# Optimization experiments

Measured on AMD Instinct MI355X. Metric: run time of the kernel, lower is better.

The kernel has to match this reference:

```python
import jax, jax.numpy as jnp
import numpy as np

B, NC, NS = 128, 32, 128          # graphs, compound atoms/graph, pocket sites/graph
NV, NSITE = B * NC, B * NS        # 4096 compound atoms, 16384 site atoms total
EV, ES = NV * 4, NSITE * 8        # edge counts (avg degree 4 / 8)
FDIM, SDIM = 82, 32               # atom feature dims
H, HS, HP, HI = 128, 128, 128, 64 # hidden_vert, hidden_site, hidden_prot, hidden_int
D, K = 3, 8                       # GNN depth (both), attention heads
P = B * NC * NS                   # 524288 site-atom pairs


def setup_inputs():
    key = jax.random.key(0)
    ks = iter(jax.random.split(key, 80))
    def nrm(shape, s=0.05):
        return jax.random.normal(next(ks), shape, jnp.float32) * s
    inp = {}
    inp['x_vert'] = jax.random.normal(next(ks), (NV, FDIM), jnp.float32)
    inp['vert_src'] = jax.random.randint(next(ks), (EV,), 0, NV)
    inp['vert_dst'] = jax.random.randint(next(ks), (EV,), 0, NV)
    inp['vert_batch'] = jnp.repeat(jnp.arange(B, dtype=jnp.int32), NC)
    inp['W_emb'] = nrm((FDIM, H)); inp['b_emb'] = jnp.zeros((H,), jnp.float32)
    inp['Wa_main'] = nrm((D, K, H, H)); inp['Wa_super'] = nrm((D, K, H, H))
    inp['Wv'] = nrm((D, K, H, H)); inp['Wb'] = nrm((D, K, H))
    inp['Wm2s'] = nrm((D, K * H, H)); inp['Ws2m'] = nrm((D, H, H))
    inp['Wsup'] = nrm((D, H, H)); inp['Wself'] = nrm((D, H, H))
    inp['Wzm1'] = nrm((D, H, H)); inp['Wzm2'] = nrm((D, H, H))
    inp['Wzs1'] = nrm((D, H, H)); inp['Wzs2'] = nrm((D, H, H))
    for tag in ('m', 's'):
        inp['Wih_' + tag] = nrm((H, 3 * H)); inp['Whh_' + tag] = nrm((H, 3 * H))
        inp['bih_' + tag] = jnp.zeros((3 * H,), jnp.float32)
        inp['bhh_' + tag] = jnp.zeros((3 * H,), jnp.float32)
    inp['x_site'] = jax.random.normal(next(ks), (NSITE, SDIM), jnp.float32)
    inp['site_src'] = jax.random.randint(next(ks), (ES,), 0, NSITE)
    inp['site_dst'] = jax.random.randint(next(ks), (ES,), 0, NSITE)
    inp['W0'] = nrm((2 * SDIM, HS)); inp['b0'] = jnp.zeros((HS,), jnp.float32)
    inp['Wconv'] = nrm((D - 1, 2 * HS, HS)); inp['bconv'] = jnp.zeros((D - 1, HS), jnp.float32)
    inp['Wout'] = nrm((SDIM + D * HS, HP)); inp['bout'] = jnp.zeros((HP,), jnp.float32)
    inp['Wis'] = nrm((7, HP, HI)); inp['bis'] = jnp.zeros((7, HI), jnp.float32)
    inp['Wic'] = nrm((7, H, HI)); inp['bic'] = jnp.zeros((7, HI), jnp.float32)
    # block-diagonal all-pairs index (every site x every compound atom within a graph)
    g = jnp.arange(B, dtype=jnp.int32)
    a = jnp.arange(NS, dtype=jnp.int32)
    c = jnp.arange(NC, dtype=jnp.int32)
    inp['idx_site'] = jnp.broadcast_to(g[:, None, None] * NS + a[None, :, None], (B, NS, NC)).reshape(-1)
    inp['idx_comp'] = jnp.broadcast_to(g[:, None, None] * NC + c[None, None, :], (B, NS, NC)).reshape(-1)
    return inp


def _leaky(x):
    return jnp.where(x > 0, x, 0.1 * x)


def _gru(x, h, Wih, Whh, bih, bhh):
    gi = x @ Wih + bih
    gh = h @ Whh + bhh
    ir, iz, inn = jnp.split(gi, 3, axis=-1)
    hr, hz, hn = jnp.split(gh, 3, axis=-1)
    r = jax.nn.sigmoid(ir + hr)
    z = jax.nn.sigmoid(iz + hz)
    n = jnp.tanh(inn + r * hn)
    return (1.0 - z) * n + z * h


def reference(x_vert, vert_src, vert_dst, vert_batch, W_emb, b_emb,
              Wa_main, Wa_super, Wv, Wb, Wm2s, Ws2m, Wsup, Wself,
              Wzm1, Wzm2, Wzs1, Wzs2,
              Wih_m, Whh_m, bih_m, bhh_m, Wih_s, Whh_s, bih_s, bhh_s,
              x_site, site_src, site_dst, W0, b0, Wconv, bconv, Wout, bout,
              Wis, bis, Wic, bic, idx_site, idx_comp):
    seg = jax.ops.segment_sum
    # ---- GraphConv_module: embedding + GWM (graph warp) iterations ----
    vert = _leaky(x_vert @ W_emb + b_emb)                      # [NV, H]
    supe = seg(vert, vert_batch, num_segments=B)               # [B, H] super node init
    for d in range(D):
        # local vertex message passing
        nei = seg(vert[vert_src], vert_dst, num_segments=NV)
        main_self = _leaky((vert + nei) @ Wself[d])
        # multi-head main -> super attention (segment softmax over each graph)
        am = jnp.tanh(jnp.einsum('nd,kde->kne', vert, Wa_main[d]))        # [K,NV,H]
        asup = jnp.tanh(jnp.einsum('bd,kde->kbe', supe, Wa_super[d]))     # [K,B,H]
        score = jnp.einsum('kne,ke->nk', am * asup[:, vert_batch], Wb[d]) # [NV,K]
        smax = jax.ops.segment_max(score, vert_batch, num_segments=B)
        e = jnp.exp(score - smax[vert_batch])
        attn = e / seg(e, vert_batch, num_segments=B)[vert_batch]         # [NV,K]
        msg = jnp.einsum('nd,kde->nke', vert, Wv[d])                      # [NV,K,H]
        m2s = seg(attn[:, :, None] * msg, vert_batch, num_segments=B)     # [B,K,H]
        main_to_super = jnp.tanh(m2s.reshape(B, K * H) @ Wm2s[d])         # [B,H]
        super_to_main = jnp.tanh(supe @ Ws2m[d])[vert_batch]              # [NV,H]
        # warp gates + shared GRU updates
        zm = jax.nn.sigmoid(main_self @ Wzm1[d] + super_to_main @ Wzm2[d])
        vert = _gru((1 - zm) * main_self + zm * super_to_main, vert, Wih_m, Whh_m, bih_m, bhh_m)
        super_self = jnp.tanh(supe @ Wsup[d])
        zs = jax.nn.sigmoid(super_self @ Wzs1[d] + main_to_super @ Wzs2[d])
        supe = _gru((1 - zs) * super_self + zs * main_to_super, supe, Wih_s, Whh_s, bih_s, bhh_s)
    # ---- AtomConv_module on protein sites ----
    h = x_site
    feats = [h]
    for i in range(D):
        nei = seg(h[site_src], site_dst, num_segments=NSITE)
        W = W0 if i == 0 else Wconv[i - 1]
        b = b0 if i == 0 else bconv[i - 1]
        h = _leaky(jnp.concatenate([h, nei], axis=-1) @ W + b)
        feats.append(h)
    site = _leaky(jnp.concatenate(feats, axis=-1) @ Wout + bout)  # [NSITE, HP]
    # ---- Interaction_pred_module: 7-head gather-multiply-reduce over pairs ----
    preds = []
    for i in range(7):
        pa = _leaky(site @ Wis[i] + bis[i])   # [NSITE, HI]
        pg = _leaky(vert @ Wic[i] + bic[i])   # [NV, HI]
        preds.append(jnp.sum(pa[idx_site] * pg[idx_comp], axis=1))  # [P]
    return jnp.stack(preds, axis=1)           # [P, 7]
```

## Files before the change

kernel.cpp:

```cpp
#include <hip/hip_runtime.h>
#include <hip/hip_bf16.h>

typedef unsigned short u16;
typedef unsigned int u32;

static constexpr int cNV = 4096, cEV = 16384, cB = 128, cNC = 32, cNS = 128;
static constexpr int cNSITE = 16384, cES = 131072;
static constexpr int cH = 128, cK8 = 8, cHI = 64;

__device__ __forceinline__ float leakyf(float x){ return x > 0.f ? x : 0.1f * x; }
__device__ __forceinline__ float sigm(float x){ return 1.f / (1.f + __expf(-x)); }

typedef __attribute__((ext_vector_type(4))) short short4v;
typedef __attribute__((ext_vector_type(4))) float f32x4;

__device__ __forceinline__ u16 f2bu(float x){
  __hip_bfloat16 h = __float2bfloat16(x);
  return *(u16*)&h;
}
__device__ __forceinline__ float bf2f(u16 u){
  __hip_bfloat16 h; *(u16*)&h = u;
  return __bfloat162float(h);
}

__global__ void zero_k(float* __restrict__ p, long n){
  long i = (long)blockIdx.x * 256 + threadIdx.x;
  if (i < n) p[i] = 0.f;
}

__global__ void cvtw_k(const float* __restrict__ src, u16* __restrict__ dst,
                       int K, int krsh, int N, int ldw, int cshift, int cs){
  long i = (long)blockIdx.x * 256 + threadIdx.x;
  int Kr = 1 << krsh;
  if (i >= (long)N * Kr) return;
  int n = (int)(i >> krsh), k = (int)(i & (Kr - 1));
  float v = 0.f;
  if (k < K) v = src[(long)k * ldw + (long)(n >> cshift) * cs + (n & ((1 << cshift) - 1))];
  dst[i] = f2bu(v);
}

struct GSegs {
  const u16* Wt[4];
  const float* bias[4];
  const float* addA[4];
  void* C[4];
  u16* C2[4];
  int nb_end[4];
  int N[4];
  int Kr[4];
  int act[4];
  int odt[4];
  int nsegs;
};

__global__ __launch_bounds__(256) void gemm_g(
    const void* __restrict__ A0, const void* __restrict__ A1,
    const void* __restrict__ A2, const void* __restrict__ A3,
    int dt0, int dt1, int dt2, int dt3,
    int k1, int k2, int k3, int K, int M,
    GSegs segs, const float* __restrict__ ep1, const float* __restrict__ ep2)
{
  __shared__ __align__(16) u16 As[64 * 136];
  __shared__ __align__(16) u16 Bs[64 * 136];
  const int t = threadIdx.x;
  const int l = t & 63, w = t >> 6;
  const int wr = w >> 1, wc = w & 1;
  const int lr = l & 15, lh = l >> 4;

  const int nwg = gridDim.x * gridDim.y;
  const int bid = blockIdx.y * gridDim.x + blockIdx.x;
  const int cpx = nwg >> 3;
  const int swz = (bid & 7) * cpx + (bid >> 3);
  const int bx = swz % gridDim.x, by = swz / gridDim.x;

  const u16* Wt = nullptr; const float* bias = nullptr; const float* addA = nullptr;
  void* C = nullptr; u16* C2 = nullptr;
  int Nn = 0, Kr = 0, act = 0, odt = 0, nb0 = 0;
  {
    int nbs = 0;
    #pragma unroll
    for (int s = 0; s < 4; s++) {
      if (s < segs.nsegs) {
        int e = segs.nb_end[s];
        if (bx >= nbs && bx < e) {
          Wt = segs.Wt[s]; bias = segs.bias[s]; addA = segs.addA[s];
          C = segs.C[s]; C2 = segs.C2[s];
          Nn = segs.N[s]; Kr = segs.Kr[s]; act = segs.act[s]; odt = segs.odt[s];
          nb0 = nbs;
        }
        nbs = e;
      }
    }
  }
  const int n0 = (bx - nb0) * 64;
  const int m0 = by * 64;
  const int w1 = k2 - k1, w2 = k3 - k2, w3 = K - k3;

  f32x4 acc[2][2];
  #pragma unroll
  for (int i = 0; i < 2; i++)
    #pragma unroll
    for (int j = 0; j < 2; j++)
      acc[i][j] = (f32x4){0.f, 0.f, 0.f, 0.f};

  const int arow = t >> 2, kq = (t & 3) * 32;
  const int bcol = t & 63, bq = (t >> 6) * 32;
  const int mg = m0 + arow;

  for (int kt = 0; kt < K; kt += 128) {
    #pragma unroll
    for (int sub = 0; sub < 4; sub++) {
      const int kg0 = kt + kq + sub * 8;
      const void* bp; int st, wseg, dt;
      if (kg0 < k1)      { bp = A0; st = 0;  wseg = k1; dt = dt0; }
      else if (kg0 < k2) { bp = A1; st = k1; wseg = w1; dt = dt1; }
      else if (kg0 < k3) { bp = A2; st = k2; wseg = w2; dt = dt2; }
      else               { bp = A3; st = k3; wseg = w3; dt = dt3; }
      uint4 v;
      if (dt == 0 && addA == nullptr && kg0 + 8 <= st + wseg) {
        v = *(const uint4*)((const u16*)bp + (long)mg * wseg + (kg0 - st));
      } else {
        float f[8];
        #pragma unroll
        for (int j = 0; j < 8; j++) {
          int kg = kg0 + j;
          float x = 0.f;
          if (kg < K) {
            long o = (long)mg * wseg + (kg - st);
            x = dt ? ((const float*)bp)[o] : bf2f(((const u16*)bp)[o]);
            if (addA != nullptr) x += addA[(long)mg * K + kg];
          }
          f[j] = x;
        }
        v.x = (u32)f2bu(f[0]) | ((u32)f2bu(f[1]) << 16);
        v.y = (u32)f2bu(f[2]) | ((u32)f2bu(f[3]) << 16);
        v.z = (u32)f2bu(f[4]) | ((u32)f2bu(f[5]) << 16);
        v.w = (u32)f2bu(f[6]) | ((u32)f2bu(f[7]) << 16);
      }
      *(uint4*)&As[arow * 136 + kq + sub * 8] = v;
    }
    #pragma unroll
    for (int sub = 0; sub < 4; sub++) {
      uint4 v = *(const uint4*)(Wt + (long)(n0 + bcol) * Kr + kt + bq + sub * 8);
      *(uint4*)&Bs[bcol * 136 + bq + sub * 8] = v;
    }
    __syncthreads();
    #pragma unroll
    for (int ks = 0; ks < 8; ks++) {
      short4v a0 = *(short4v*)&As[(wr * 32 + 0 * 16 + lr) * 136 + ks * 16 + lh * 4];
      short4v a1 = *(short4v*)&As[(wr * 32 + 1 * 16 + lr) * 136 + ks * 16 + lh * 4];
      short4v b0 = *(short4v*)&Bs[(wc * 32 + 0 * 16 + lr) * 136 + ks * 16 + lh * 4];
      short4v b1 = *(short4v*)&Bs[(wc * 32 + 1 * 16 + lr) * 136 + ks * 16 + lh * 4];
      acc[0][0] = __builtin_amdgcn_mfma_f32_16x16x16bf16_1k(a0, b0, acc[0][0], 0, 0, 0);
      acc[0][1] = __builtin_amdgcn_mfma_f32_16x16x16bf16_1k(a0, b1, acc[0][1], 0, 0, 0);
      acc[1][0] = __builtin_amdgcn_mfma_f32_16x16x16bf16_1k(a1, b0, acc[1][0], 0, 0, 0);
      acc[1][1] = __builtin_amdgcn_mfma_f32_16x16x16bf16_1k(a1, b1, acc[1][1], 0, 0, 0);
    }
    __syncthreads();
  }
  #pragma unroll
  for (int ri = 0; ri < 2; ri++) {
    #pragma unroll
    for (int ci = 0; ci < 2; ci++) {
      int col = n0 + wc * 32 + ci * 16 + lr;
      float bv = (bias != nullptr) ? bias[col] : 0.f;
      #pragma unroll
      for (int e = 0; e < 4; e++) {
        int row = m0 + wr * 32 + ri * 16 + lh * 4 + e;
        float v = acc[ri][ci][e] + bv;
        if (act == 1) v = leakyf(v);
        else if (act == 2) v = tanhf(v);
        else if (act == 3) v = sigm(v);
        else if (act == 4) {
          int b = row >> 5;
          float zm = sigm(v + ep1[b * 128 + col]);
          float msv = bf2f(((const u16*)A0)[(long)row * k1 + col]);
          v = (1.f - zm) * msv + zm * ep2[b * 128 + col];
        }
        long o = (long)row * Nn + col;
        if (odt == 0) ((float*)C)[o] = v;
        else if (odt == 1) ((u16*)C)[o] = f2bu(v);
        else { ((float*)C)[o] = v; C2[o] = f2bu(v); }
      }
    }
  }
}

__global__ void supe_init_k(const float* __restrict__ vert, float* __restrict__ supe){
  int b = blockIdx.x, c = threadIdx.x;
  float s = 0.f;
  for (int i = 0; i < cNC; i++) s += vert[(b * cNC + i) * cH + c];
  supe[b * cH + c] = s;
}

__global__ void scatter_vert_k(const float* __restrict__ vert, const int* __restrict__ src,
                               const int* __restrict__ dst, float* __restrict__ nei){
  int idx = blockIdx.x * 256 + threadIdx.x;
  if (idx >= cEV * cH) return;
  int e = idx >> 7, c = idx & 127;
  atomicAdd(&nei[dst[e] * cH + c], vert[src[e] * cH + c]);
}

__global__ __launch_bounds__(256) void supe_pre_k(
    const float* __restrict__ supe,
    const float* __restrict__ Wa_super_d, const float* __restrict__ Ws2m_d,
    const float* __restrict__ Wzm2_d, const float* __restrict__ Wsup_d,
    const float* __restrict__ Whh_s, const float* __restrict__ bhh_s,
    float* __restrict__ asup, float* __restrict__ s2m, float* __restrict__ s2mz,
    float* __restrict__ sself, float* __restrict__ gh_s)
{
  __shared__ float srow[cH];
  __shared__ float s2ml[cH];
  int b = blockIdx.x, t = threadIdx.x;
  if (t < cH) srow[t] = supe[b * cH + t];
  __syncthreads();
  for (int j = 0; j < 4; j++) {
    int c = t + j * 256;
    int head = c >> 7, e = c & 127;
    const float* Wp = Wa_super_d + head * 16384 + e;
    float s = 0.f;
    for (int d2 = 0; d2 < cH; d2++) s += srow[d2] * Wp[d2 * 128];
    asup[b * 1024 + c] = tanhf(s);
  }
  if (t < cH) {
    float s = 0.f;
    for (int d2 = 0; d2 < cH; d2++) s += srow[d2] * Ws2m_d[d2 * 128 + t];
    float v = tanhf(s);
    s2ml[t] = v; s2m[b * cH + t] = v;
  } else {
    int c = t - cH;
    float s = 0.f;
    for (int d2 = 0; d2 < cH; d2++) s += srow[d2] * Wsup_d[d2 * 128 + c];
    sself[b * cH + c] = tanhf(s);
  }
  {
    int c = t;
    float s = 0.f;
    for (int d2 = 0; d2 < cH; d2++) s += srow[d2] * Whh_s[d2 * 384 + c];
    gh_s[b * 384 + c] = s + bhh_s[c];
    if (t < cH) {
      int c2 = 256 + t;
      float s2 = 0.f;
      for (int d2 = 0; d2 < cH; d2++) s2 += srow[d2] * Whh_s[d2 * 384 + c2];
      gh_s[b * 384 + c2] = s2 + bhh_s[c2];
    }
  }
  __syncthreads();
  if (t < cH) {
    float s = 0.f;
    for (int d2 = 0; d2 < cH; d2++) s += s2ml[d2] * Wzm2_d[d2 * 128 + t];
    s2mz[b * cH + t] = s;
  }
}

__global__ __launch_bounds__(256) void attn_k(
    const float* __restrict__ am, const float* __restrict__ asup,
    const float* __restrict__ Wb_d, float* __restrict__ attn)
{
  __shared__ float pw[1024];
  __shared__ float sc[cNC][cK8];
  int b = blockIdx.x, t = threadIdx.x;
  for (int j = 0; j < 4; j++) {
    int c = t + j * 256;
    pw[c] = asup[b * 1024 + c] * Wb_d[c];
  }
  __syncthreads();
  int nl = t >> 3, k = t & 7;
  int n = b * cNC + nl;
  const float* ar = am + (long)n * 1024 + k * 128;
  const float* pr = pw + k * 128;
  float s = 0.f;
  for (int e = 0; e < 128; e++) s += ar[e] * pr[e];
  sc[nl][k] = s;
  __syncthreads();
  float mx = -1e30f;
  for (int i = 0; i < cNC; i++) mx = fmaxf(mx, sc[i][k]);
  float den = 0.f;
  for (int i = 0; i < cNC; i++) den += __expf(sc[i][k] - mx);
  attn[n * cK8 + k] = __expf(s - mx) / den;
}

__global__ __launch_bounds__(256) void m2s_k(
    const float* __restrict__ attn, const float* __restrict__ msg,
    const float* __restrict__ Wm2s_d, float* __restrict__ mts)
{
  __shared__ float m2s[1024];
  __shared__ float at[cNC][cK8];
  int b = blockIdx.x, t = threadIdx.x;
  at[t >> 3][t & 7] = attn[(b * cNC + (t >> 3)) * cK8 + (t & 7)];
  __syncthreads();
  for (int j = 0; j < 4; j++) {
    int c = t + j * 256;
    int k = c >> 7;
    float s = 0.f;
    for (int i = 0; i < cNC; i++) s += at[i][k] * msg[(long)(b * cNC + i) * 1024 + c];
    m2s[c] = s;
  }
  __syncthreads();
  if (t < cH) {
    float s = 0.f;
    for (int j = 0; j < 1024; j++) s += m2s[j] * Wm2s_d[j * 128 + t];
    mts[b * cH + t] = tanhf(s);
  }
}

__global__ void ew_gru_k(const u16* __restrict__ gi, const u16* __restrict__ gh,
                         float* __restrict__ h, u16* __restrict__ hb){
  int idx = blockIdx.x * 256 + threadIdx.x;
  if (idx >= cNV * cH) return;
  int n = idx >> 7, c = idx & 127;
  const u16* gir = gi + (long)n * 384;
  const u16* ghr = gh + (long)n * 384;
  float r = sigm(bf2f(gir[c]) + bf2f(ghr[c]));
  float z = sigm(bf2f(gir[128 + c]) + bf2f(ghr[128 + c]));
  float nn = tanhf(bf2f(gir[256 + c]) + r * bf2f(ghr[256 + c]));
  float v = (1.f - z) * nn + z * h[idx];
  h[idx] = v;
  hb[idx] = f2bu(v);
}

__global__ __launch_bounds__(128) void super_upd_k(
    const float* __restrict__ sself, const float* __restrict__ mts,
    const float* __restrict__ gh_s,
    const float* __restrict__ Wzs1_d, const float* __restrict__ Wzs2_d,
    const float* __restrict__ Wih_s, const float* __restrict__ bih_s,
    float* __restrict__ supe)
{
  __shared__ float ss[cH], mt[cH], xs[cH], sr[cH];
  int b = blockIdx.x, t = threadIdx.x;
  ss[t] = sself[b * cH + t];
  mt[t] = mts[b * cH + t];
  sr[t] = supe[b * cH + t];
  __syncthreads();
  float s1 = 0.f, s2 = 0.f;
  for (int d2 = 0; d2 < cH; d2++) {
    s1 += ss[d2] * Wzs1_d[d2 * 128 + t];
    s2 += mt[d2] * Wzs2_d[d2 * 128 + t];
  }
  float zs = sigm(s1 + s2);
  xs[t] = (1.f - zs) * ss[t] + zs * mt[t];
  __syncthreads();
  float g0 = 0.f, g1 = 0.f, g2 = 0.f;
  for (int d2 = 0; d2 < cH; d2++) {
    float x = xs[d2];
    g0 += x * Wih_s[d2 * 384 + t];
    g1 += x * Wih_s[d2 * 384 + 128 + t];
    g2 += x * Wih_s[d2 * 384 + 256 + t];
  }
  g0 += bih_s[t]; g1 += bih_s[128 + t]; g2 += bih_s[256 + t];
  float r = sigm(g0 + gh_s[b * 384 + t]);
  float z = sigm(g1 + gh_s[b * 384 + 128 + t]);
  float nn = tanhf(g2 + r * gh_s[b * 384 + 256 + t]);
  supe[b * cH + t] = (1.f - z) * nn + z * sr[t];
}

__global__ void scatter_site_k(const float* __restrict__ h, const int* __restrict__ src,
                               const int* __restrict__ dst, float* __restrict__ nei,
                               int dshift){
  long idx = (long)blockIdx.x * 256 + threadIdx.x;
  int din = 1 << dshift;
  if (idx >= (long)cES * din) return;
  int e = (int)(idx >> dshift);
  int c = (int)(idx & (din - 1));
  atomicAdd(&nei[(long)dst[e] * din + c], h[(long)src[e] * din + c]);
}

__global__ void scatter_site_b_k(const u16* __restrict__ h, const int* __restrict__ src,
                                 const int* __restrict__ dst, float* __restrict__ nei){
  long idx = (long)blockIdx.x * 256 + threadIdx.x;
  if (idx >= (long)cES * 128) return;
  int e = (int)(idx >> 7);
  int c = (int)(idx & 127);
  atomicAdd(&nei[(long)dst[e] * 128 + c], bf2f(h[(long)src[e] * 128 + c]));
}

__global__ __launch_bounds__(256) void pair_k(
    const u16* __restrict__ pa, const u16* __restrict__ pg, float* __restrict__ out)
{
  __shared__ float pal[cNS][cHI];
  __shared__ float pgl[cNC][cHI + 1];
  int g = blockIdx.x, i = blockIdx.y;
  int t = threadIdx.x;
  for (int l = t; l < cNS * cHI; l += 256) {
    int s = l >> 6, hh = l & 63;
    pal[s][hh] = bf2f(pa[(long)(g * cNS + s) * 448 + i * 64 + hh]);
  }
  for (int l = t; l < cNC * cHI; l += 256) {
    int c = l >> 6, hh = l & 63;
    pgl[c][hh] = bf2f(pg[(long)(g * cNC + c) * 448 + i * 64 + hh]);
  }
  __syncthreads();
  for (int o = t; o < cNS * cNC; o += 256) {
    int s = o >> 5, c = o & 31;
    float sum = 0.f;
    #pragma unroll 8
    for (int hh = 0; hh < cHI; hh++) sum += pal[s][hh] * pgl[c][hh];
    long p = (long)g * (cNS * cNC) + o;
    out[p * 7 + i] = sum;
  }
}

extern "C" void kernel_launch(void* const* d_in, const int* in_sizes, int n_in,
                              void* d_out, int out_size, void* d_ws, size_t ws_size,
                              hipStream_t stream) {
  constexpr long OFF_VERT = 0;
  constexpr long OFF_SUPE = 524288;
  constexpr long OFF_SITE = 1064960;
  constexpr long OFF_ATTN = 3162112;
  constexpr long OFF_ASUP = 3194880;
  constexpr long OFF_S2M = 3325952;
  constexpr long OFF_S2MZ = 3342336;
  constexpr long OFF_SSELF = 3358720;
  constexpr long OFF_GHS = 3375104;
  constexpr long OFF_MTS = 3424256;
  constexpr long OFF_NEI = 3440640;
  constexpr long OFF_TMPA = 3964928;
  constexpr long OFF_MS = 4489216;
  constexpr long OFF_ZMP = 5013504;
  constexpr long OFF_XGRU = 5537792;
  constexpr long OFF_GHM = 6062080;
  constexpr long OFF_GIM = 7634944;
  constexpr long OFF_AM = 9207808;
  constexpr long OFF_MSG = 13402112;
  constexpr long OFF_H1 = 17596416;
  constexpr long OFF_H2 = 19693568;
  constexpr long OFF_H3 = 21790720;
  constexpr long WS_FLOATS = 23887872;
  if (ws_size < (size_t)WS_FLOATS * 4) return;

  constexpr long WT_EMB = 0;
  constexpr long WT_SELF = 16384;
  constexpr long WT_AMAIN = 65536;
  constexpr long WT_V = 458752;
  constexpr long WT_HHM = 851968;
  constexpr long WT_ZM1 = 901120;
  constexpr long WT_IHM = 950272;
  constexpr long WT_W0 = 999424;
  constexpr long WT_CONV = 1015808;
  constexpr long WT_OUT = 1081344;
  constexpr long WT_IS = 1146880;
  constexpr long WT_IC = 1204224;

  const float* x_vert  = (const float*)d_in[0];
  const int*   vsrc    = (const int*)d_in[1];
  const int*   vdst    = (const int*)d_in[2];
  const float* W_emb   = (const float*)d_in[4];
  const float* b_emb   = (const float*)d_in[5];
  const float* Wa_main = (const float*)d_in[6];
  const float* Wa_super= (const float*)d_in[7];
  const float* Wv      = (const float*)d_in[8];
  const float* Wb      = (const float*)d_in[9];
  const float* Wm2s    = (const float*)d_in[10];
  const float* Ws2m    = (const float*)d_in[11];
  const float* Wsup    = (const float*)d_in[12];
  const float* Wself   = (const float*)d_in[13];
  const float* Wzm1    = (const float*)d_in[14];
  const float* Wzm2    = (const float*)d_in[15];
  const float* Wzs1    = (const float*)d_in[16];
  const float* Wzs2    = (const float*)d_in[17];
  const float* Wih_m   = (const float*)d_in[18];
  const float* Whh_m   = (const float*)d_in[19];
  const float* bih_m   = (const float*)d_in[20];
  const float* bhh_m   = (const float*)d_in[21];
  const float* Wih_s   = (const float*)d_in[22];
  const float* Whh_s   = (const float*)d_in[23];
  const float* bih_s   = (const float*)d_in[24];
  const float* bhh_s   = (const float*)d_in[25];
  const float* x_site  = (const float*)d_in[26];
  const int*   ssrc    = (const int*)d_in[27];
  const int*   sdst    = (const int*)d_in[28];
  const float* W0      = (const float*)d_in[29];
  const float* b0      = (const float*)d_in[30];
  const float* Wconv   = (const float*)d_in[31];
  const float* bconv   = (const float*)d_in[32];
  const float* Wout    = (const float*)d_in[33];
  const float* bout    = (const float*)d_in[34];
  const float* Wis     = (const float*)d_in[35];
  const float* bis     = (const float*)d_in[36];
  const float* Wic     = (const float*)d_in[37];
  const float* bic     = (const float*)d_in[38];
  float* out = (float*)d_out;

  float* ws = (float*)d_ws;
  float* vert  = ws + OFF_VERT;
  float* supe  = ws + OFF_SUPE;
  float* attn  = ws + OFF_ATTN;
  float* asup  = ws + OFF_ASUP;
  float* s2m   = ws + OFF_S2M;
  float* s2mz  = ws + OFF_S2MZ;
  float* sself = ws + OFF_SSELF;
  float* gh_s  = ws + OFF_GHS;
  float* mts   = ws + OFF_MTS;
  float* nei   = ws + OFF_NEI;
  float* am    = ws + OFF_AM;
  float* msg   = ws + OFF_MSG;
  float* nei_s = ws + OFF_AM;

  u16* vert_b = (u16*)(ws + OFF_ZMP);
  u16* ms_b   = (u16*)(ws + OFF_MS);
  u16* xgru_b = (u16*)(ws + OFF_XGRU);
  u16* ghm_b  = (u16*)(ws + OFF_GHM);
  u16* gim_b  = (u16*)(ws + OFF_GHM + 786432);
  u16* h1b    = (u16*)(ws + OFF_H1);
  u16* h2b    = (u16*)(ws + OFF_H2);
  u16* h3b    = (u16*)(ws + OFF_H3);
  u16* site_b = (u16*)(ws + OFF_SITE);
  u16* pa_b   = (u16*)(ws + OFF_MSG);
  u16* pg_b   = (u16*)(ws + OFF_GIM);
  u16* wbuf   = (u16*)(ws + OFF_H3 + 1048576);

  auto zero = [&](float* p, long n){
    zero_k<<<dim3((unsigned)((n + 255) / 256)), 256, 0, stream>>>(p, n);
  };
  auto cvtw = [&](const float* src, long wt_off, int K, int krsh, int N,
                  int ldw, int cshift, int cs){
    long tot = (long)N << krsh;
    cvtw_k<<<dim3((unsigned)((tot + 255) / 256)), 256, 0, stream>>>(
        src, wbuf + wt_off, K, krsh, N, ldw, cshift, cs);
  };
  auto gemm1 = [&](const void* A0, int dt0, const void* A1, int dt1,
                   const void* A2, int dt2, const void* A3, int dt3,
                   int k1, int k2, int k3, int K, int M,
                   long wt_off, int Kr, const float* bias,
                   void* C, u16* C2, int N, int act, int odt,
                   const float* addA = nullptr,
                   const float* ep1 = nullptr, const float* ep2 = nullptr){
    GSegs s{};
    s.Wt[0] = wbuf + wt_off; s.bias[0] = bias; s.addA[0] = addA;
    s.C[0] = C; s.C2[0] = C2;
    s.nb_end[0] = N / 64; s.N[0] = N; s.Kr[0] = Kr; s.act[0] = act; s.odt[0] = odt;
    s.nsegs = 1;
    dim3 g(N / 64, M / 64);
    gemm_g<<<g, 256, 0, stream>>>(A0, A1, A2, A3, dt0, dt1, dt2, dt3,
                                  k1, k2, k3, K, M, s, ep1, ep2);
  };

  cvtw(W_emb, WT_EMB, 82, 7, 128, 128, 30, 0);
  cvtw(Wself, WT_SELF, 128, 7, 384, 128, 7, 16384);
  cvtw(Wa_main, WT_AMAIN, 128, 7, 3072, 128, 7, 16384);
  cvtw(Wv, WT_V, 128, 7, 3072, 128, 7, 16384);
  cvtw(Whh_m, WT_HHM, 128, 7, 384, 384, 30, 0);
  cvtw(Wzm1, WT_ZM1, 128, 7, 384, 128, 7, 16384);
  cvtw(Wih_m, WT_IHM, 128, 7, 384, 384, 30, 0);
  cvtw(W0, WT_W0, 64, 7, 128, 128, 30, 0);
  cvtw(Wconv, WT_CONV, 256, 8, 256, 128, 7, 32768);
  cvtw(Wout, WT_OUT, 416, 9, 128, 128, 30, 0);
  cvtw(Wis, WT_IS, 128, 7, 448, 64, 6, 8192);
  cvtw(Wic, WT_IC, 128, 7, 448, 64, 6, 8192);

  gemm1(x_vert, 1, x_vert, 1, x_vert, 1, x_vert, 1, 82, 82, 82, 82, cNV,
        WT_EMB, 128, b_emb, vert, vert_b, 128, 1, 2);
  supe_init_k<<<cB, 128, 0, stream>>>(vert, supe);

  for (int d = 0; d < 3; d++) {
    const float* Wa_super_d = Wa_super + (long)d * 131072;
    const float* Wb_d = Wb + (long)d * 1024;
    const float* Wm2s_d = Wm2s + (long)d * 131072;
    const float* Ws2m_d = Ws2m + (long)d * 16384;
    const float* Wsup_d = Wsup + (long)d * 16384;
    const float* Wzm2_d = Wzm2 + (long)d * 16384;
    const float* Wzs1_d = Wzs1 + (long)d * 16384;
    const float* Wzs2_d = Wzs2 + (long)d * 16384;

    zero(nei, (long)cNV * cH);
    scatter_vert_k<<<(cEV * cH) / 256, 256, 0, stream>>>(vert, vsrc, vdst, nei);

    {
      GSegs s{};
      s.Wt[0] = wbuf + WT_SELF + (long)d * 16384;  s.bias[0] = nullptr;
      s.addA[0] = nei;     s.C[0] = ms_b;  s.C2[0] = nullptr;
      s.N[0] = 128;  s.Kr[0] = 128; s.act[0] = 1; s.odt[0] = 1; s.nb_end[0] = 2;
      s.Wt[1] = wbuf + WT_AMAIN + (long)d * 131072; s.bias[1] = nullptr;
      s.addA[1] = nullptr; s.C[1] = am;    s.C2[1] = nullptr;
      s.N[1] = 1024; s.Kr[1] = 128; s.act[1] = 2; s.odt[1] = 0; s.nb_end[1] = 18;
      s.Wt[2] = wbuf + WT_V + (long)d * 131072;     s.bias[2] = nullptr;
      s.addA[2] = nullptr; s.C[2] = msg;   s.C2[2] = nullptr;
      s.N[2] = 1024; s.Kr[2] = 128; s.act[2] = 0; s.odt[2] = 0; s.nb_end[2] = 34;
      s.Wt[3] = wbuf + WT_HHM;                      s.bias[3] = bhh_m;
      s.addA[3] = nullptr; s.C[3] = ghm_b; s.C2[3] = nullptr;
      s.N[3] = 384;  s.Kr[3] = 128; s.act[3] = 0; s.odt[3] = 1; s.nb_end[3] = 40;
      s.nsegs = 4;
      dim3 g(40, cNV / 64);
      gemm_g<<<g, 256, 0, stream>>>(vert_b, vert_b, vert_b, vert_b, 0, 0, 0, 0,
                                    128, 128, 128, 128, cNV, s, nullptr, nullptr);
    }
    supe_pre_k<<<cB, 256, 0, stream>>>(supe, Wa_super_d, Ws2m_d, Wzm2_d, Wsup_d,
                                       Whh_s, bhh_s, asup, s2m, s2mz, sself, gh_s);
    attn_k<<<cB, 256, 0, stream>>>(am, asup, Wb_d, attn);
    m2s_k<<<cB, 256, 0, stream>>>(attn, msg, Wm2s_d, mts);
    gemm1(ms_b, 0, ms_b, 0, ms_b, 0, ms_b, 0, 128, 128, 128, 128, cNV,
          WT_ZM1 + (long)d * 16384, 128, nullptr, xgru_b, nullptr, 128, 4, 1,
          nullptr, s2mz, s2m);
    gemm1(xgru_b, 0, xgru_b, 0, xgru_b, 0, xgru_b, 0, 128, 128, 128, 128, cNV,
          WT_IHM, 128, bih_m, gim_b, nullptr, 384, 0, 1);
    ew_gru_k<<<(cNV * cH) / 256, 256, 0, stream>>>(gim_b, ghm_b, vert, vert_b);
    super_upd_k<<<cB, 128, 0, stream>>>(sself, mts, gh_s, Wzs1_d, Wzs2_d,
                                        Wih_s, bih_s, supe);
  }

  zero(nei_s, (long)cNSITE * 32);
  scatter_site_k<<<((long)cES * 32) / 256, 256, 0, stream>>>(x_site, ssrc, sdst, nei_s, 5);
  gemm1(x_site, 1, nei_s, 1, nei_s, 1, nei_s, 1, 32, 64, 64, 64, cNSITE,
        WT_W0, 128, b0, h1b, nullptr, 128, 1, 1);
  zero(nei_s, (long)cNSITE * 128);
  scatter_site_b_k<<<((long)cES * 128) / 256, 256, 0, stream>>>(h1b, ssrc, sdst, nei_s);
  gemm1(h1b, 0, nei_s, 1, nei_s, 1, nei_s, 1, 128, 256, 256, 256, cNSITE,
        WT_CONV, 256, bconv, h2b, nullptr, 128, 1, 1);
  zero(nei_s, (long)cNSITE * 128);
  scatter_site_b_k<<<((long)cES * 128) / 256, 256, 0, stream>>>(h2b, ssrc, sdst, nei_s);
  gemm1(h2b, 0, nei_s, 1, nei_s, 1, nei_s, 1, 128, 256, 256, 256, cNSITE,
        WT_CONV + 32768, 256, bconv + 128, h3b, nullptr, 128, 1, 1);
  gemm1(x_site, 1, h1b, 0, h2b, 0, h3b, 0, 32, 160, 288, 416, cNSITE,
        WT_OUT, 512, bout, site_b, nullptr, 128, 1, 1);

  gemm1(site_b, 0, site_b, 0, site_b, 0, site_b, 0, 128, 128, 128, 128, cNSITE,
        WT_IS, 128, bis, pa_b, nullptr, 448, 1, 1);
  gemm1(vert_b, 0, vert_b, 0, vert_b, 0, vert_b, 0, 128, 128, 128, 128, cNV,
        WT_IC, 128, bic, pg_b, nullptr, 448, 1, 1);
  pair_k<<<dim3(cB, 7), 256, 0, stream>>>(pa_b, pg_b, out);
}
```

Before: 892.2 us.

## Replace atomic edge scatters with CSR-sorted gather aggregation

Builds CSR adjacency (count, scan, fill) for the compound and site graphs once per call, then replaces the zero-plus-atomicAdd scatter kernels with per-destination-row gather kernels. Site neighbor sums are now written in bf16, which halves that buffer's traffic and feeds the GEMMs a bf16 operand. This removes heavy float atomic contention and the zeroing passes, but adds several small preprocessing launches and a serial single-block scan. Summation order within a row now depends on atomic fill order, and the neighbor sums lose precision from bf16 storage.

```diff
diff --git a/kernel.cpp b/kernel.cpp
--- a/kernel.cpp
+++ b/kernel.cpp
@@ -23,9 +23,70 @@
   return __bfloat162float(h);
 }
 
-__global__ void zero_k(float* __restrict__ p, long n){
-  long i = (long)blockIdx.x * 256 + threadIdx.x;
-  if (i < n) p[i] = 0.f;
+__global__ void zero_i_k(int* __restrict__ p, int n){
+  int i = blockIdx.x * 256 + threadIdx.x;
+  if (i < n) p[i] = 0;
+}
+__global__ void copy_i_k(const int* __restrict__ s, int* __restrict__ d, int n){
+  int i = blockIdx.x * 256 + threadIdx.x;
+  if (i < n) d[i] = s[i];
+}
+__global__ void count_k(const int* __restrict__ dst, int* __restrict__ cnt, int ne){
+  int i = blockIdx.x * 256 + threadIdx.x;
+  if (i < ne) atomicAdd(&cnt[dst[i]], 1);
+}
+__global__ void scan_k(const int* __restrict__ cnt, int* __restrict__ off, int n){
+  __shared__ int part[256];
+  int t = threadIdx.x;
+  int chunk = n >> 8;
+  int base = t * chunk;
+  int s = 0;
+  for (int j = 0; j < chunk; j++) s += cnt[base + j];
+  part[t] = s;
+  __syncthreads();
+  for (int d = 1; d < 256; d <<= 1) {
+    int v = (t >= d) ? part[t - d] : 0;
+    __syncthreads();
+    part[t] += v;
+    __syncthreads();
+  }
+  int run = (t == 0) ? 0 : part[t - 1];
+  for (int j = 0; j < chunk; j++) { off[base + j] = run; run += cnt[base + j]; }
+  if (t == 255) off[n] = run;
+}
+__global__ void fill_k(const int* __restrict__ src, const int* __restrict__ dst,
+                       int* __restrict__ cur, int* __restrict__ perm, int ne){
+  int i = blockIdx.x * 256 + threadIdx.x;
+  if (i < ne) {
+    int p = atomicAdd(&cur[dst[i]], 1);
+    perm[p] = src[i];
+  }
+}
+
+__global__ void gather128_f_k(const float* __restrict__ h, const int* __restrict__ off,
+                              const int* __restrict__ perm, float* __restrict__ nei){
+  int row = blockIdx.x, t = threadIdx.x;
+  int b = off[row], e = off[row + 1];
+  float s = 0.f;
+  for (int i = b; i < e; i++) s += h[(long)perm[i] * 128 + t];
+  nei[(long)row * 128 + t] = s;
+}
+__global__ void gather128_b_k(const u16* __restrict__ h, const int* __restrict__ off,
+                              const int* __restrict__ perm, u16* __restrict__ nei){
+  int row = blockIdx.x, t = threadIdx.x;
+  int b = off[row], e = off[row + 1];
+  float s = 0.f;
+  for (int i = b; i < e; i++) s += bf2f(h[(long)perm[i] * 128 + t]);
+  nei[(long)row * 128 + t] = f2bu(s);
+}
+__global__ void gather32_k(const float* __restrict__ h, const int* __restrict__ off,
+                           const int* __restrict__ perm, u16* __restrict__ nei){
+  int t = threadIdx.x;
+  int row = blockIdx.x * 8 + (t >> 5), c = t & 31;
+  int b = off[row], e = off[row + 1];
+  float s = 0.f;
+  for (int i = b; i < e; i++) s += h[(long)perm[i] * 32 + c];
+  nei[(long)row * 32 + c] = f2bu(s);
 }
 
 __global__ void cvtw_k(const float* __restrict__ src, u16* __restrict__ dst,
@@ -193,14 +254,6 @@
   supe[b * cH + c] = s;
 }
 
-__global__ void scatter_vert_k(const float* __restrict__ vert, const int* __restrict__ src,
-                               const int* __restrict__ dst, float* __restrict__ nei){
-  int idx = blockIdx.x * 256 + threadIdx.x;
-  if (idx >= cEV * cH) return;
-  int e = idx >> 7, c = idx & 127;
-  atomicAdd(&nei[dst[e] * cH + c], vert[src[e] * cH + c]);
-}
-
 __global__ __launch_bounds__(256) void supe_pre_k(
     const float* __restrict__ supe,
     const float* __restrict__ Wa_super_d, const float* __restrict__ Ws2m_d,
@@ -352,26 +405,6 @@
   float z = sigm(g1 + gh_s[b * 384 + 128 + t]);
   float nn = tanhf(g2 + r * gh_s[b * 384 + 256 + t]);
   supe[b * cH + t] = (1.f - z) * nn + z * sr[t];
-}
-
-__global__ void scatter_site_k(const float* __restrict__ h, const int* __restrict__ src,
-                               const int* __restrict__ dst, float* __restrict__ nei,
-                               int dshift){
-  long idx = (long)blockIdx.x * 256 + threadIdx.x;
-  int din = 1 << dshift;
-  if (idx >= (long)cES * din) return;
-  int e = (int)(idx >> dshift);
-  int c = (int)(idx & (din - 1));
-  atomicAdd(&nei[(long)dst[e] * din + c], h[(long)src[e] * din + c]);
-}
-
-__global__ void scatter_site_b_k(const u16* __restrict__ h, const int* __restrict__ src,
-                                 const int* __restrict__ dst, float* __restrict__ nei){
-  long idx = (long)blockIdx.x * 256 + threadIdx.x;
-  if (idx >= (long)cES * 128) return;
-  int e = (int)(idx >> 7);
-  int c = (int)(idx & 127);
-  atomicAdd(&nei[(long)dst[e] * 128 + c], bf2f(h[(long)src[e] * 128 + c]));
 }
 
 __global__ __launch_bounds__(256) void pair_k(
@@ -494,7 +527,6 @@
   float* nei   = ws + OFF_NEI;
   float* am    = ws + OFF_AM;
   float* msg   = ws + OFF_MSG;
-  float* nei_s = ws + OFF_AM;
 
   u16* vert_b = (u16*)(ws + OFF_ZMP);
   u16* ms_b   = (u16*)(ws + OFF_MS);
@@ -505,13 +537,19 @@
   u16* h2b    = (u16*)(ws + OFF_H2);
   u16* h3b    = (u16*)(ws + OFF_H3);
   u16* site_b = (u16*)(ws + OFF_SITE);
+  u16* nei_sb = (u16*)(ws + OFF_AM);
   u16* pa_b   = (u16*)(ws + OFF_MSG);
   u16* pg_b   = (u16*)(ws + OFF_GIM);
   u16* wbuf   = (u16*)(ws + OFF_H3 + 1048576);
 
-  auto zero = [&](float* p, long n){
-    zero_k<<<dim3((unsigned)((n + 255) / 256)), 256, 0, stream>>>(p, n);
-  };
+  int* iws   = (int*)(ws + OFF_TMPA);
+  int* voff  = iws;
+  int* vcur  = iws + 8192;
+  int* vperm = iws + 16384;
+  int* soff  = iws + 32768;
+  int* scur  = iws + 57344;
+  int* sperm = iws + 81920;
+
   auto cvtw = [&](const float* src, long wt_off, int K, int krsh, int N,
                   int ldw, int cshift, int cs){
     long tot = (long)N << krsh;
@@ -535,6 +573,17 @@
                                   k1, k2, k3, K, M, s, ep1, ep2);
   };
 
+  zero_i_k<<<16, 256, 0, stream>>>(vcur, cNV);
+  count_k<<<cEV / 256, 256, 0, stream>>>(vdst, vcur, cEV);
+  scan_k<<<1, 256, 0, stream>>>(vcur, voff, cNV);
+  copy_i_k<<<16, 256, 0, stream>>>(voff, vcur, cNV);
+  fill_k<<<cEV / 256, 256, 0, stream>>>(vsrc, vdst, vcur, vperm, cEV);
+  zero_i_k<<<64, 256, 0, stream>>>(scur, cNSITE);
+  count_k<<<cES / 256, 256, 0, stream>>>(sdst, scur, cES);
+  scan_k<<<1, 256, 0, stream>>>(scur, soff, cNSITE);
+  copy_i_k<<<64, 256, 0, stream>>>(soff, scur, cNSITE);
+  fill_k<<<cES / 256, 256, 0, stream>>>(ssrc, sdst, scur, sperm, cES);
+
   cvtw(W_emb, WT_EMB, 82, 7, 128, 128, 30, 0);
   cvtw(Wself, WT_SELF, 128, 7, 384, 128, 7, 16384);
   cvtw(Wa_main, WT_AMAIN, 128, 7, 3072, 128, 7, 16384);
@@ -562,8 +611,7 @@
     const float* Wzs1_d = Wzs1 + (long)d * 16384;
     const float* Wzs2_d = Wzs2 + (long)d * 16384;
 
-    zero(nei, (long)cNV * cH);
-    scatter_vert_k<<<(cEV * cH) / 256, 256, 0, stream>>>(vert, vsrc, vdst, nei);
+    gather128_f_k<<<cNV, 128, 0, stream>>>(vert, voff, vperm, nei);
 
     {
       GSegs s{};
@@ -598,17 +646,14 @@
                                         Wih_s, bih_s, supe);
   }
 
-  zero(nei_s, (long)cNSITE * 32);
-  scatter_site_k<<<((long)cES * 32) / 256, 256, 0, stream>>>(x_site, ssrc, sdst, nei_s, 5);
-  gemm1(x_site, 1, nei_s, 1, nei_s, 1, nei_s, 1, 32, 64, 64, 64, cNSITE,
+  gather32_k<<<cNSITE / 8, 256, 0, stream>>>(x_site, soff, sperm, nei_sb);
+  gemm1(x_site, 1, nei_sb, 0, nei_sb, 0, nei_sb, 0, 32, 64, 64, 64, cNSITE,
         WT_W0, 128, b0, h1b, nullptr, 128, 1, 1);
-  zero(nei_s, (long)cNSITE * 128);
-  scatter_site_b_k<<<((long)cES * 128) / 256, 256, 0, stream>>>(h1b, ssrc, sdst, nei_s);
-  gemm1(h1b, 0, nei_s, 1, nei_s, 1, nei_s, 1, 128, 256, 256, 256, cNSITE,
+  gather128_b_k<<<cNSITE, 128, 0, stream>>>(h1b, soff, sperm, nei_sb);
+  gemm1(h1b, 0, nei_sb, 0, nei_sb, 0, nei_sb, 0, 128, 256, 256, 256, cNSITE,
         WT_CONV, 256, bconv, h2b, nullptr, 128, 1, 1);
-  zero(nei_s, (long)cNSITE * 128);
-  scatter_site_b_k<<<((long)cES * 128) / 256, 256, 0, stream>>>(h2b, ssrc, sdst, nei_s);
-  gemm1(h2b, 0, nei_s, 1, nei_s, 1, nei_s, 1, 128, 256, 256, 256, cNSITE,
+  gather128_b_k<<<cNSITE, 128, 0, stream>>>(h2b, soff, sperm, nei_sb);
+  gemm1(h2b, 0, nei_sb, 0, nei_sb, 0, nei_sb, 0, 128, 256, 256, 256, cNSITE,
         WT_CONV + 32768, 256, bconv + 128, h3b, nullptr, 128, 1, 1);
   gemm1(x_site, 1, h1b, 0, h2b, 0, h3b, 0, 32, 160, 288, 416, cNSITE,
         WT_OUT, 512, bout, site_b, nullptr, 128, 1, 1);
```

Result: faster. 833.0 us (-6.6%).
